# Optimization experiments

Measured on AMD Instinct MI355X. Metric: run time of the kernel, lower is better.

The kernel has to match this reference:

```python
import jax, jax.numpy as jnp
import numpy as np

B, N, E = 2, 2048, 1024   # batch, seq_len, embed_dim (= hidden_dim)
H, HD = 16, 64            # num_heads, head_dim


def setup_inputs() -> dict:
    key = jax.random.key(0)
    ks = jax.random.split(key, 6)
    w = lambda k: jax.random.normal(k, (E, E), jnp.float32) * 0.02
    return {
        "x": jax.random.normal(ks[0], (B, N, E), jnp.float32),
        "Wq": w(ks[1]), "bq": jnp.zeros((E,), jnp.float32),
        "Wk": w(ks[2]), "bk": jnp.zeros((E,), jnp.float32),
        "Wv": w(ks[3]), "bv": jnp.zeros((E,), jnp.float32),
        "Wu": w(ks[4]), "bu": jnp.zeros((E,), jnp.float32),
        "Wo": w(ks[5]), "bo": jnp.zeros((E,), jnp.float32),
        "ln_g": jnp.ones((E,), jnp.float32),
        "ln_b": jnp.zeros((E,), jnp.float32),
    }


def reference(x, Wq, bq, Wk, bk, Wv, bv, Wu, bu, Wo, bo, ln_g, ln_b):
    # projections (torch Linear: x @ W.T + b)
    q = x @ Wq.T + bq
    k = x @ Wk.T + bk
    v = jax.nn.silu(x @ Wv.T + bv)   # uv_act = swish
    u = jax.nn.silu(x @ Wu.T + bu)
    # split heads: [B, N, H*HD] -> [B, H, N, HD]
    split = lambda t: t.reshape(B, N, H, HD).transpose(0, 2, 1, 3)
    q, k, v = split(q), split(k), split(v)
    # non-softmax attention: ReLU on scaled energy (no causal mask)
    energy = jnp.einsum("bhnd,bhmd->bhnm", q, k) / jnp.float32(np.sqrt(HD))
    energy = jax.nn.relu(energy)
    out = jnp.einsum("bhnm,bhmd->bhnd", energy, v)
    # merge heads: [B, H, N, HD] -> [B, N, H*HD]
    out = out.transpose(0, 2, 1, 3).reshape(B, N, H * HD)
    # layernorm over hidden_dim
    mu = out.mean(-1, keepdims=True)
    var = out.var(-1, keepdims=True)
    out = (out - mu) * jax.lax.rsqrt(var + 1e-5) * ln_g + ln_b
    # gate and output projection
    out = u * out
    return out @ Wo.T + bo
```

## Files before the change

kernel.cpp:

```cpp
#include <hip/hip_runtime.h>
#include <stdint.h>

typedef unsigned short u16;
typedef __attribute__((ext_vector_type(8))) short short8;
typedef __attribute__((ext_vector_type(4))) short short4v;
typedef __attribute__((ext_vector_type(4))) float floatx4;
typedef __attribute__((ext_vector_type(4))) int intx4;

#define B_ 2
#define N_ 2048
#define E_ 1024
#define H_ 16
#define HD_ 64
#define M_TOT (B_ * N_)

__device__ __forceinline__ float bf2f(u16 h) {
    union { unsigned u; float f; } c; c.u = ((unsigned)h) << 16; return c.f;
}
__device__ __forceinline__ u16 f2bf(float f) {
    union { float f; unsigned u; } c; c.f = f;
    unsigned r = c.u + 0x7FFFu + ((c.u >> 16) & 1u);
    return (u16)(r >> 16);
}
__device__ __forceinline__ float silu_f(float x) { return x / (1.f + __expf(-x)); }

template <typename T> __device__ __forceinline__ void store_out(T* p, float v);
template <> __device__ __forceinline__ void store_out<u16>(u16* p, float v)    { *p = f2bf(v); }
template <> __device__ __forceinline__ void store_out<float>(float* p, float v) { *p = v; }

__device__ __forceinline__ void gll16(const void* g, void* l) {
    __builtin_amdgcn_global_load_lds(
        (const __attribute__((address_space(1))) void*)g,
        (__attribute__((address_space(3))) void*)l,
        16, 0, 0);
}

__launch_bounds__(256, 4)
__global__ void cvt6(const float* __restrict__ s0, const float* __restrict__ s1,
                     const float* __restrict__ s2, const float* __restrict__ s3,
                     const float* __restrict__ s4, const float* __restrict__ s5,
                     u16* __restrict__ d0, u16* __restrict__ d1,
                     u16* __restrict__ d2, u16* __restrict__ d3,
                     u16* __restrict__ d4, u16* __restrict__ d5)
{
    const int z = blockIdx.z;
    if (z > 0 && blockIdx.x >= E_ * E_ / 2048) return;
    const float* src = (z == 0) ? s0 : (z == 1) ? s1 : (z == 2) ? s2
                     : (z == 3) ? s3 : (z == 4) ? s4 : s5;
    u16* dst         = (z == 0) ? d0 : (z == 1) ? d1 : (z == 2) ? d2
                     : (z == 3) ? d3 : (z == 4) ? d4 : d5;
    const int i = (blockIdx.x * 256 + threadIdx.x) * 8;
    floatx4 a = *(const floatx4*)(src + i);
    floatx4 b = *(const floatx4*)(src + i + 4);
    union { u16 h[8]; intx4 v; } o;
    o.h[0] = f2bf(a[0]); o.h[1] = f2bf(a[1]); o.h[2] = f2bf(a[2]); o.h[3] = f2bf(a[3]);
    o.h[4] = f2bf(b[0]); o.h[5] = f2bf(b[1]); o.h[6] = f2bf(b[2]); o.h[7] = f2bf(b[3]);
    *(intx4*)(dst + i) = o.v;
}

template <typename OutT>
__launch_bounds__(256, 2)
__global__ void gemm4(const u16* __restrict__ A,
                      const u16* __restrict__ W0, const u16* __restrict__ W1,
                      const u16* __restrict__ W2, const u16* __restrict__ W3,
                      const float* __restrict__ bi0, const float* __restrict__ bi1,
                      const float* __restrict__ bi2, const float* __restrict__ bi3,
                      OutT* __restrict__ O0, OutT* __restrict__ O1,
                      OutT* __restrict__ O2, OutT* __restrict__ O3,
                      int actmask, int K)
{
    __shared__ u16 a_lds[128 * 32];
    __shared__ u16 b_lds[128 * 32];

    const int z = blockIdx.z;
    const u16* W    = (z == 0) ? W0 : (z == 1) ? W1 : (z == 2) ? W2 : W3;
    const float* Bi = (z == 0) ? bi0 : (z == 1) ? bi1 : (z == 2) ? bi2 : bi3;
    OutT* Out       = (z == 0) ? O0 : (z == 1) ? O1 : (z == 2) ? O2 : O3;
    const bool act = (actmask >> z) & 1;

    const int t    = threadIdx.x;
    const int wave = t >> 6, lane = t & 63, quad = lane >> 4, l16 = lane & 15;
    const int wm = wave >> 1, wn = wave & 1;
    const int m0 = blockIdx.y * 128;
    const int n0 = blockIdx.x * 128;

    floatx4 acc[4][4];
    const floatx4 fz = {0.f, 0.f, 0.f, 0.f};
    for (int i = 0; i < 4; i++)
        for (int j = 0; j < 4; j++) acc[i][j] = fz;

    const int ar = t >> 2;
    const int ac = (t & 3) * 8;
    const u16* Ag0 = A + (size_t)(m0 + ar) * K + ac;
    const u16* Ag1 = A + (size_t)(m0 + 64 + ar) * K + ac;
    const u16* Bg0 = W + (size_t)(n0 + ar) * K + ac;
    const u16* Bg1 = W + (size_t)(n0 + 64 + ar) * K + ac;
    u16* al0 = a_lds + wave * 512;
    u16* al1 = a_lds + 2048 + wave * 512;
    u16* bl0 = b_lds + wave * 512;
    u16* bl1 = b_lds + 2048 + wave * 512;

    for (int k0 = 0; k0 < K; k0 += 32) {
        __syncthreads();
        gll16(Ag0 + k0, al0);
        gll16(Ag1 + k0, al1);
        gll16(Bg0 + k0, bl0);
        gll16(Bg1 + k0, bl1);
        __syncthreads();

        short8 af[4], bfr[4];
        for (int i = 0; i < 4; i++)
            af[i]  = *(const short8*)&a_lds[(wm * 64 + i * 16 + l16) * 32 + quad * 8];
        for (int j = 0; j < 4; j++)
            bfr[j] = *(const short8*)&b_lds[(wn * 64 + j * 16 + l16) * 32 + quad * 8];
        for (int i = 0; i < 4; i++)
            for (int j = 0; j < 4; j++)
                acc[i][j] = __builtin_amdgcn_mfma_f32_16x16x32_bf16(af[i], bfr[j], acc[i][j], 0, 0, 0);
    }

    float bias_v[4];
    for (int j = 0; j < 4; j++) bias_v[j] = Bi[n0 + wn * 64 + j * 16 + l16];

    for (int i = 0; i < 4; i++) {
        const int row = m0 + wm * 64 + i * 16 + quad * 4;
        for (int j = 0; j < 4; j++) {
            const int col = n0 + wn * 64 + j * 16 + l16;
            for (int r = 0; r < 4; r++) {
                float v = acc[i][j][r] + bias_v[j];
                if (act) v = silu_f(v);
                store_out<OutT>(&Out[(size_t)(row + r) * E_ + col], v);
            }
        }
    }
}

__launch_bounds__(256, 4)
__global__ void vtrans(const u16* __restrict__ V, u16* __restrict__ VT)
{
    __shared__ u16 ts[64 * 72];
    const int bh = blockIdx.y;
    const int b = bh >> 4, h = bh & 15;
    const int n0 = blockIdx.x * 64;
    const int t = threadIdx.x;
    const int r = t >> 2, seg = (t & 3) * 16;

    const u16* src = V + ((size_t)b * N_ + n0 + r) * E_ + h * HD_ + seg;
    intx4 x0 = *(const intx4*)(src);
    intx4 x1 = *(const intx4*)(src + 8);
    *(intx4*)&ts[r * 72 + seg]     = x0;
    *(intx4*)&ts[r * 72 + seg + 8] = x1;
    __syncthreads();

    union { u16 h[16]; intx4 v[2]; } buf;
    for (int j = 0; j < 16; j++) buf.h[j] = ts[(seg + j) * 72 + r];
    u16* dst = VT + ((size_t)bh * HD_ + r) * N_ + n0 + seg;
    *(intx4*)(dst)     = buf.v[0];
    *(intx4*)(dst + 8) = buf.v[1];
}

#define LQ 72
#define KSPLIT 2
#define KCHUNK (N_ / KSPLIT)

__launch_bounds__(256, 2)
__global__ void attn(const u16* __restrict__ Q, const u16* __restrict__ Kk,
                     const u16* __restrict__ VT,
                     float* __restrict__ Oa0, float* __restrict__ Oa1)
{
    __shared__ u16 k_lds[64 * LQ];
    __shared__ u16 vt_lds[64 * LQ];
    __shared__ u16 s_lds[4 * 32 * LQ];

    const int bh = blockIdx.y;
    const int b = bh >> 4, h = bh & 15;
    const int z = blockIdx.z;
    float* __restrict__ Oa = (z == 0) ? Oa0 : Oa1;
    const int key_base = z * KCHUNK;

    const int t = threadIdx.x;
    const int wave = t >> 6, lane = t & 63, quad = lane >> 4, l16 = lane & 15;
    const int q0 = blockIdx.x * 128 + wave * 32;
    const size_t base = (size_t)b * N_ * E_ + h * HD_;

    short8 aq[2][2];
    for (int mi = 0; mi < 2; mi++)
        for (int ks = 0; ks < 2; ks++)
            aq[mi][ks] = *(const short8*)(Q + base + (size_t)(q0 + mi * 16 + l16) * E_ + ks * 32 + quad * 8);

    floatx4 o[2][4];
    const floatx4 fz = {0.f, 0.f, 0.f, 0.f};
    for (int mi = 0; mi < 2; mi++)
        for (int n = 0; n < 4; n++) o[mi][n] = fz;

    const int srow = t >> 2;
    const int sseg = (t & 3) * 16;
    const u16* Ksrc = Kk + base + (size_t)(key_base + srow) * E_ + sseg;
    const u16* Vsrc = VT + ((size_t)bh * HD_ + srow) * N_ + key_base + sseg;

    u16* sw = &s_lds[wave * 32 * LQ];

    for (int kt = 0; kt < KCHUNK / 64; kt++) {
        __syncthreads();
        intx4 k0v = *(const intx4*)(Ksrc + (size_t)(kt * 64) * E_);
        intx4 k1v = *(const intx4*)(Ksrc + (size_t)(kt * 64) * E_ + 8);
        intx4 v0v = *(const intx4*)(Vsrc + kt * 64);
        intx4 v1v = *(const intx4*)(Vsrc + kt * 64 + 8);
        *(intx4*)&k_lds[srow * LQ + sseg]      = k0v;
        *(intx4*)&k_lds[srow * LQ + sseg + 8]  = k1v;
        *(intx4*)&vt_lds[srow * LQ + sseg]     = v0v;
        *(intx4*)&vt_lds[srow * LQ + sseg + 8] = v1v;
        __syncthreads();

        short8 bk[4][2];
        for (int n = 0; n < 4; n++)
            for (int ks = 0; ks < 2; ks++)
                bk[n][ks] = *(const short8*)&k_lds[(n * 16 + l16) * LQ + ks * 32 + quad * 8];

        for (int mi = 0; mi < 2; mi++) {
            for (int n = 0; n < 4; n++) {
                floatx4 s = fz;
                for (int ks = 0; ks < 2; ks++)
                    s = __builtin_amdgcn_mfma_f32_16x16x32_bf16(aq[mi][ks], bk[n][ks], s, 0, 0, 0);
                for (int r = 0; r < 4; r++) {
                    float v = s[r] * 0.125f;
                    v = v > 0.f ? v : 0.f;
                    sw[(mi * 16 + quad * 4 + r) * LQ + n * 16 + l16] = f2bf(v);
                }
            }
        }

        for (int ks = 0; ks < 2; ks++) {
            short8 bv[4];
            for (int n = 0; n < 4; n++)
                bv[n] = *(const short8*)&vt_lds[(n * 16 + l16) * LQ + ks * 32 + quad * 8];
            for (int mi = 0; mi < 2; mi++) {
                short8 as = *(const short8*)&sw[(mi * 16 + l16) * LQ + ks * 32 + quad * 8];
                for (int n = 0; n < 4; n++)
                    o[mi][n] = __builtin_amdgcn_mfma_f32_16x16x32_bf16(as, bv[n], o[mi][n], 0, 0, 0);
            }
        }
    }

    for (int mi = 0; mi < 2; mi++)
        for (int n = 0; n < 4; n++)
            for (int r = 0; r < 4; r++)
                Oa[(size_t)(b * N_ + q0 + mi * 16 + quad * 4 + r) * E_ + h * HD_ + n * 16 + l16] = o[mi][n][r];
}

__launch_bounds__(256, 4)
__global__ void ln_gate(const float* __restrict__ A0, const float* __restrict__ A1,
                        const u16* __restrict__ U,
                        const float* __restrict__ G, const float* __restrict__ Bb,
                        u16* __restrict__ Out)
{
    const int row = blockIdx.x;
    const int t = threadIdx.x;
    const floatx4 v0 = *(const floatx4*)(A0 + (size_t)row * E_ + t * 4);
    const floatx4 v1 = *(const floatx4*)(A1 + (size_t)row * E_ + t * 4);
    floatx4 v;
    for (int i = 0; i < 4; i++) v[i] = v0[i] + v1[i];
    float s  = v[0] + v[1] + v[2] + v[3];
    float ss = v[0] * v[0] + v[1] * v[1] + v[2] * v[2] + v[3] * v[3];
    for (int off = 32; off; off >>= 1) {
        s  += __shfl_down(s, off, 64);
        ss += __shfl_down(ss, off, 64);
    }
    __shared__ float red[8];
    const int wave = t >> 6, lane = t & 63;
    if (lane == 0) { red[wave] = s; red[4 + wave] = ss; }
    __syncthreads();
    const float S  = red[0] + red[1] + red[2] + red[3];
    const float SS = red[4] + red[5] + red[6] + red[7];
    const float mu  = S * (1.f / E_);
    const float var = SS * (1.f / E_) - mu * mu;
    const float rstd = rsqrtf(var + 1e-5f);

    short4v outv;
    for (int i = 0; i < 4; i++) {
        const int e = t * 4 + i;
        float y = (v[i] - mu) * rstd * G[e] + Bb[e];
        y *= bf2f(U[(size_t)row * E_ + e]);
        outv[i] = (short)f2bf(y);
    }
    *(short4v*)(Out + (size_t)row * E_ + t * 4) = outv;
}

extern "C" void kernel_launch(void* const* d_in, const int* in_sizes, int n_in,
                              void* d_out, int out_size, void* d_ws, size_t ws_size,
                              hipStream_t stream)
{
    const float* x   = (const float*)d_in[0];
    const float* Wq  = (const float*)d_in[1];
    const float* bq  = (const float*)d_in[2];
    const float* Wk  = (const float*)d_in[3];
    const float* bk  = (const float*)d_in[4];
    const float* Wv  = (const float*)d_in[5];
    const float* bv  = (const float*)d_in[6];
    const float* Wu  = (const float*)d_in[7];
    const float* bu  = (const float*)d_in[8];
    const float* Wo  = (const float*)d_in[9];
    const float* bo  = (const float*)d_in[10];
    const float* lng = (const float*)d_in[11];
    const float* lnb = (const float*)d_in[12];

    char* ws = (char*)d_ws;
    u16*  qw  = (u16*)(ws);
    u16*  kw  = (u16*)(ws + 8388608);
    u16*  vw  = (u16*)(ws + 16777216);
    u16*  uw  = (u16*)(ws + 25165824);
    float* aw = (float*)(ws + 33554432);
    u16*  xb  = (u16*)(ws + 50331648);
    u16*  vt  = (u16*)(ws + 50331648);
    u16*  wbq = (u16*)(ws + 58720256);
    u16*  wbk = (u16*)(ws + 60817408);
    u16*  wbv = (u16*)(ws + 62914560);
    u16*  wbu = (u16*)(ws + 65011712);
    u16*  wbo = (u16*)(ws + 67108864);
    u16*  gw  = (u16*)(ws);

    float* out = (float*)d_out;

    const dim3 blk(256, 1, 1);

    cvt6<<<dim3(M_TOT * E_ / 2048, 1, 6), blk, 0, stream>>>(
        x, Wq, Wk, Wv, Wu, Wo, xb, wbq, wbk, wbv, wbu, wbo);
    gemm4<u16><<<dim3(8, 32, 4), blk, 0, stream>>>(xb, wbq, wbk, wbv, wbu,
                                                   bq, bk, bv, bu,
                                                   qw, kw, vw, uw, 0xC, E_);
    vtrans<<<dim3(N_ / 64, B_ * H_, 1), blk, 0, stream>>>(vw, vt);
    attn<<<dim3(N_ / 128, B_ * H_, KSPLIT), blk, 0, stream>>>(qw, kw, vt, aw, out);
    ln_gate<<<dim3(M_TOT, 1, 1), blk, 0, stream>>>(aw, out, uw, lng, lnb, gw);
    gemm4<float><<<dim3(8, 32, 1), blk, 0, stream>>>(gw, wbo, wbo, wbo, wbo,
                                                     bo, bo, bo, bo,
                                                     out, out, out, out, 0x0, E_);
}
```

Before: 238.0 us.

## Keep attention scores in registers via transposed MFMA, drop LDS score staging

```diff
diff --git a/kernel.cpp b/kernel.cpp
--- a/kernel.cpp
+++ b/kernel.cpp
@@ -33,6 +33,29 @@
         (const __attribute__((address_space(1))) void*)g,
         (__attribute__((address_space(3))) void*)l,
         16, 0, 0);
+}
+
+#if __has_builtin(__builtin_amdgcn_mfma_f32_16x16x16bf16_1k)
+__device__ __forceinline__ floatx4 mfma16(short4v a, short4v b, floatx4 c) {
+    return __builtin_amdgcn_mfma_f32_16x16x16bf16_1k(a, b, c, 0, 0, 0);
+}
+#else
+__device__ __forceinline__ floatx4 mfma16(short4v a, short4v b, floatx4 c) {
+    floatx4 d;
+    asm volatile("v_mfma_f32_16x16x16_bf16 %0, %1, %2, %3\n\ts_nop 3"
+                 : "=v"(d) : "v"(a), "v"(b), "v"(c));
+    return d;
+}
+#endif
+
+__device__ __forceinline__ short4v relu_pack(floatx4 s) {
+    union { float f; unsigned u; } c0, c1, c2, c3;
+    c0.f = fmaxf(s[0], 0.f); c1.f = fmaxf(s[1], 0.f);
+    c2.f = fmaxf(s[2], 0.f); c3.f = fmaxf(s[3], 0.f);
+    unsigned lo = __builtin_amdgcn_perm(c1.u + 0x8000u, c0.u + 0x8000u, 0x07060302);
+    unsigned hi = __builtin_amdgcn_perm(c3.u + 0x8000u, c2.u + 0x8000u, 0x07060302);
+    union { unsigned v[2]; short4v s4; } r; r.v[0] = lo; r.v[1] = hi;
+    return r.s4;
 }
 
 __launch_bounds__(256, 4)
@@ -67,7 +90,7 @@
                       const float* __restrict__ bi2, const float* __restrict__ bi3,
                       OutT* __restrict__ O0, OutT* __restrict__ O1,
                       OutT* __restrict__ O2, OutT* __restrict__ O3,
-                      int actmask, int K)
+                      int actmask, int scalemask, int K)
 {
     __shared__ u16 a_lds[128 * 32];
     __shared__ u16 b_lds[128 * 32];
@@ -77,6 +100,7 @@
     const float* Bi = (z == 0) ? bi0 : (z == 1) ? bi1 : (z == 2) ? bi2 : bi3;
     OutT* Out       = (z == 0) ? O0 : (z == 1) ? O1 : (z == 2) ? O2 : O3;
     const bool act = (actmask >> z) & 1;
+    const float osc = ((scalemask >> z) & 1) ? 0.125f : 1.0f;
 
     const int t    = threadIdx.x;
     const int wave = t >> 6, lane = t & 63, quad = lane >> 4, l16 = lane & 15;
@@ -128,6 +152,7 @@
             for (int r = 0; r < 4; r++) {
                 float v = acc[i][j][r] + bias_v[j];
                 if (act) v = silu_f(v);
+                v *= osc;
                 store_out<OutT>(&Out[(size_t)(row + r) * E_ + col], v);
             }
         }
@@ -162,14 +187,13 @@
 #define KSPLIT 2
 #define KCHUNK (N_ / KSPLIT)
 
-__launch_bounds__(256, 2)
+__launch_bounds__(256, 4)
 __global__ void attn(const u16* __restrict__ Q, const u16* __restrict__ Kk,
                      const u16* __restrict__ VT,
                      float* __restrict__ Oa0, float* __restrict__ Oa1)
 {
     __shared__ u16 k_lds[64 * LQ];
     __shared__ u16 vt_lds[64 * LQ];
-    __shared__ u16 s_lds[4 * 32 * LQ];
 
     const int bh = blockIdx.y;
     const int b = bh >> 4, h = bh & 15;
@@ -196,8 +220,6 @@
     const int sseg = (t & 3) * 16;
     const u16* Ksrc = Kk + base + (size_t)(key_base + srow) * E_ + sseg;
     const u16* Vsrc = VT + ((size_t)bh * HD_ + srow) * N_ + key_base + sseg;
-
-    u16* sw = &s_lds[wave * 32 * LQ];
 
     for (int kt = 0; kt < KCHUNK / 64; kt++) {
         __syncthreads();
@@ -211,32 +233,19 @@
         *(intx4*)&vt_lds[srow * LQ + sseg + 8] = v1v;
         __syncthreads();
 
-        short8 bk[4][2];
-        for (int n = 0; n < 4; n++)
-            for (int ks = 0; ks < 2; ks++)
-                bk[n][ks] = *(const short8*)&k_lds[(n * 16 + l16) * LQ + ks * 32 + quad * 8];
-
-        for (int mi = 0; mi < 2; mi++) {
-            for (int n = 0; n < 4; n++) {
-                floatx4 s = fz;
-                for (int ks = 0; ks < 2; ks++)
-                    s = __builtin_amdgcn_mfma_f32_16x16x32_bf16(aq[mi][ks], bk[n][ks], s, 0, 0, 0);
-                for (int r = 0; r < 4; r++) {
-                    float v = s[r] * 0.125f;
-                    v = v > 0.f ? v : 0.f;
-                    sw[(mi * 16 + quad * 4 + r) * LQ + n * 16 + l16] = f2bf(v);
-                }
-            }
-        }
-
-        for (int ks = 0; ks < 2; ks++) {
-            short8 bv[4];
-            for (int n = 0; n < 4; n++)
-                bv[n] = *(const short8*)&vt_lds[(n * 16 + l16) * LQ + ks * 32 + quad * 8];
+        for (int n = 0; n < 4; n++) {
+            short8 ka0 = *(const short8*)&k_lds[(n * 16 + l16) * LQ + quad * 8];
+            short8 ka1 = *(const short8*)&k_lds[(n * 16 + l16) * LQ + 32 + quad * 8];
+            short4v bv[4];
+            for (int nd = 0; nd < 4; nd++)
+                bv[nd] = *(const short4v*)&vt_lds[(nd * 16 + l16) * LQ + n * 16 + quad * 4];
+
             for (int mi = 0; mi < 2; mi++) {
-                short8 as = *(const short8*)&sw[(mi * 16 + l16) * LQ + ks * 32 + quad * 8];
-                for (int n = 0; n < 4; n++)
-                    o[mi][n] = __builtin_amdgcn_mfma_f32_16x16x32_bf16(as, bv[n], o[mi][n], 0, 0, 0);
+                floatx4 st = __builtin_amdgcn_mfma_f32_16x16x32_bf16(ka0, aq[mi][0], fz, 0, 0, 0);
+                st = __builtin_amdgcn_mfma_f32_16x16x32_bf16(ka1, aq[mi][1], st, 0, 0, 0);
+                short4v sa = relu_pack(st);
+                for (int nd = 0; nd < 4; nd++)
+                    o[mi][nd] = mfma16(sa, bv[nd], o[mi][nd]);
             }
         }
     }
@@ -326,11 +335,11 @@
         x, Wq, Wk, Wv, Wu, Wo, xb, wbq, wbk, wbv, wbu, wbo);
     gemm4<u16><<<dim3(8, 32, 4), blk, 0, stream>>>(xb, wbq, wbk, wbv, wbu,
                                                    bq, bk, bv, bu,
-                                                   qw, kw, vw, uw, 0xC, E_);
+                                                   qw, kw, vw, uw, 0xC, 0x1, E_);
     vtrans<<<dim3(N_ / 64, B_ * H_, 1), blk, 0, stream>>>(vw, vt);
     attn<<<dim3(N_ / 128, B_ * H_, KSPLIT), blk, 0, stream>>>(qw, kw, vt, aw, out);
     ln_gate<<<dim3(M_TOT, 1, 1), blk, 0, stream>>>(aw, out, uw, lng, lnb, gw);
     gemm4<float><<<dim3(8, 32, 1), blk, 0, stream>>>(gw, wbo, wbo, wbo, wbo,
                                                      bo, bo, bo, bo,
-                                                     out, out, out, out, 0x0, E_);
-}
+                                                     out, out, out, out, 0x0, 0x0, E_);
+}
```

Measured after the change: 235.9 us. Within noise of the previous version (-0.9%).
